# Performance work log

Measured on AMD Instinct MI355X. Metric: run time of the kernel, lower is better.

## Reference

```python
import jax, jax.numpy as jnp
import numpy as np

N_NODES = 100000
N_EDGES = 1600000
NFEAT, NHID, NCLASS = 64, 128, 32


def _glorot(key, shape):
    fan_in, fan_out = shape[0], shape[1]
    lim = np.sqrt(6.0 / (fan_in + fan_out))
    return jax.random.uniform(key, shape, jnp.float32, -lim, lim)


def setup_inputs() -> dict:
    key = jax.random.key(0)
    ks = jax.random.split(key, 12)
    x = jax.random.normal(ks[0], (N_NODES, NFEAT), jnp.float32)
    edge_idx = jax.random.randint(ks[1], (2, N_EDGES), 0, N_NODES, jnp.int64)
    edge_weight = jax.random.uniform(ks[2], (N_EDGES,), jnp.float32)
    return {
        "x": x,
        "edge_idx": edge_idx,
        "edge_weight": edge_weight,
        # SAGEConv 1: out = mean_agg(x) @ Wl1 + b1 + x @ Wr1
        "Wl1": _glorot(ks[3], (NFEAT, NHID)),
        "Wr1": _glorot(ks[4], (NFEAT, NHID)),
        "b1": jnp.zeros((NHID,), jnp.float32),
        # SAGEConv 2
        "Wl2": _glorot(ks[5], (NHID, NHID)),
        "Wr2": _glorot(ks[6], (NHID, NHID)),
        "b2": jnp.zeros((NHID,), jnp.float32),
        # fc head: Linear(nhid, nclass) -> Linear(nclass, 1)
        "Wfc1": _glorot(ks[7], (NHID, NCLASS)),
        "bfc1": jnp.zeros((NCLASS,), jnp.float32),
        "Wfc2": _glorot(ks[8], (NCLASS, 1)),
        "bfc2": jnp.zeros((1,), jnp.float32),
    }


def _sage_conv(x, src, dst, Wl, Wr, b, n_nodes):
    # mean aggregation of source features at destination nodes
    msg_sum = jax.ops.segment_sum(x[src], dst, num_segments=n_nodes)  # [N, d]
    deg = jax.ops.segment_sum(jnp.ones((src.shape[0], 1), x.dtype), dst,
                              num_segments=n_nodes)                    # [N, 1]
    mean = msg_sum / jnp.maximum(deg, 1.0)
    return mean @ Wl + b + x @ Wr


def reference(x, edge_idx, edge_weight, Wl1, Wr1, b1, Wl2, Wr2, b2,
              Wfc1, bfc1, Wfc2, bfc2):
    n_nodes = x.shape[0]
    src, dst = edge_idx[0], edge_idx[1]
    # dropout is identity in eval mode (training=False)
    h = _sage_conv(x, src, dst, Wl1, Wr1, b1, n_nodes)   # [N, nhid]
    h = _sage_conv(h, src, dst, Wl2, Wr2, b2, n_nodes)   # [N, nhid]
    h = h @ Wfc1 + bfc1                                   # [N, nclass]
    out = h @ Wfc2 + bfc2                                 # [N, 1]
    return out
```

## Files before the change

### kernel.cpp

```cpp
#include <hip/hip_runtime.h>

#define S_SHIFT 9
#define S_NODES 512
#define CAP     10240
#define CHUNK   4096
#define EPT     8
#define NREP    4

__global__ __launch_bounds__(512) void prep_kernel(
    const float* __restrict__ x,
    const int* __restrict__ src, const int* __restrict__ dst,
    int E, int N, int B,
    int* __restrict__ cursor, unsigned* __restrict__ bucket,
    const float* __restrict__ Wl1, const float* __restrict__ Wr1, const float* __restrict__ b1,
    const float* __restrict__ Wl2, const float* __restrict__ Wr2, const float* __restrict__ b2,
    const float* __restrict__ Wfc1, const float* __restrict__ bfc1,
    const float* __restrict__ Wfc2, const float* __restrict__ bfc2,
    float* __restrict__ ga, float2* __restrict__ gbc, float* __restrict__ c01)
{
    __shared__ unsigned stage[CHUNK];
    __shared__ unsigned char bn8[CHUNK];
    __shared__ int hist[256], scan[256], obase[256], lcur[256], lbase[256];
    __shared__ float wv[192], uu[128], vl2[128], vr2[128], w2[32];
    int t = threadIdx.x;
    int l = t & 63;
    int w = t >> 6;

    if (t < 32) w2[t] = Wfc2[t];
    __syncthreads();
    for (int j = 0; j < 16; ++j) {
        int i = w + 8 * j;
        float p = (l < 32) ? Wfc1[i * 32 + l] * w2[l] : 0.f;
        for (int m = 16; m; m >>= 1) p += __shfl_xor(p, m);
        if (l == 0) uu[i] = p;
    }
    __syncthreads();
    for (int j = 0; j < 16; ++j) {
        int i = w + 8 * j;
        float ua = uu[l], ub = uu[64 + l];
        float pa = Wl2[i * 128 + l] * ua + Wl2[i * 128 + 64 + l] * ub;
        float pb = Wr2[i * 128 + l] * ua + Wr2[i * 128 + 64 + l] * ub;
        for (int m = 32; m; m >>= 1) { pa += __shfl_xor(pa, m); pb += __shfl_xor(pb, m); }
        if (l == 0) { vl2[i] = pa; vr2[i] = pb; }
    }
    __syncthreads();
    for (int j = 0; j < 8; ++j) {
        int i = w + 8 * j;
        float l1a = Wl1[i * 128 + l], l1b = Wl1[i * 128 + 64 + l];
        float r1a = Wr1[i * 128 + l], r1b = Wr1[i * 128 + 64 + l];
        float La = vl2[l], Lb = vl2[64 + l], Ra = vr2[l], Rb = vr2[64 + l];
        float pc = l1a * La + l1b * Lb;
        float pb = l1a * Ra + l1b * Rb + r1a * La + r1b * Lb;
        float pa = r1a * Ra + r1b * Rb;
        for (int m = 32; m; m >>= 1) {
            pa += __shfl_xor(pa, m); pb += __shfl_xor(pb, m); pc += __shfl_xor(pc, m);
        }
        if (l == 0) { wv[i] = pa; wv[64 + i] = pb; wv[128 + i] = pc; }
    }
    if (blockIdx.x == 0 && w == 7) {
        float p0 = b1[l] * vr2[l] + b1[64 + l] * vr2[64 + l]
                 + b2[l] * uu[l] + b2[64 + l] * uu[64 + l];
        if (l < 32) p0 += bfc1[l] * w2[l];
        float p1 = b1[l] * vl2[l] + b1[64 + l] * vl2[64 + l];
        for (int m = 32; m; m >>= 1) { p0 += __shfl_xor(p0, m); p1 += __shfl_xor(p1, m); }
        if (l == 0) { c01[0] = p0 + bfc2[0]; c01[1] = p1; }
    }

    {
        int e0 = blockIdx.x * CHUNK;
        int cnt = E - e0; if (cnt > CHUNK) cnt = CHUNK;
        int sd[EPT], ss[EPT];
        if (t < 256) hist[t] = 0;
        __syncthreads();
        for (int k = 0; k < EPT; ++k) {
            int i = t + k * 512;
            if (i < cnt) {
                sd[k] = dst[e0 + i];
                ss[k] = src[e0 + i];
                atomicAdd(&hist[sd[k] >> S_SHIFT], 1);
            }
        }
        __syncthreads();
        if (t < 256) scan[t] = hist[t];
        __syncthreads();
        for (int off = 1; off < 256; off <<= 1) {
            int tmp = 0;
            if (t < 256 && t >= off) tmp = scan[t - off];
            __syncthreads();
            if (t < 256) scan[t] += tmp;
            __syncthreads();
        }
        if (t < 256) {
            int ob = scan[t] - hist[t];
            obase[t] = ob;
            lcur[t] = ob;
            if (t < B && hist[t] > 0) lbase[t] = atomicAdd(&cursor[t], hist[t]);
        }
        __syncthreads();
        for (int k = 0; k < EPT; ++k) {
            int i = t + k * 512;
            if (i < cnt) {
                int bb = sd[k] >> S_SHIFT;
                int pos = atomicAdd(&lcur[bb], 1);
                stage[pos] = ((unsigned)ss[k] << S_SHIFT) | (unsigned)(sd[k] & (S_NODES - 1));
                bn8[pos] = (unsigned char)bb;
            }
        }
        __syncthreads();
        for (int i = t; i < cnt; i += 512) {
            int bb = bn8[i];
            bucket[(size_t)bb * CAP + (unsigned)(lbase[bb] + (i - obase[bb]))] = stage[i];
        }
    }

    {
        int fp = l & 15, sub = l >> 4;
        float4 wa4 = ((const float4*)wv)[fp];
        float4 wb4 = ((const float4*)wv)[16 + fp];
        float4 wc4 = ((const float4*)wv)[32 + fp];
        const float4* x4 = (const float4*)x;
        int Q = (N + 3) >> 2;
        int stride = gridDim.x * 8;
        for (int qd = blockIdx.x * 8 + w; qd < Q; qd += stride) {
            int node = qd * 4 + sub;
            float a = 0.f, b = 0.f, c = 0.f;
            if (node < N) {
                float4 v = x4[(size_t)node * 16 + fp];
                a = v.x * wa4.x + v.y * wa4.y + v.z * wa4.z + v.w * wa4.w;
                b = v.x * wb4.x + v.y * wb4.y + v.z * wb4.z + v.w * wb4.w;
                c = v.x * wc4.x + v.y * wc4.y + v.z * wc4.z + v.w * wc4.w;
            }
            for (int m = 8; m; m >>= 1) {
                a += __shfl_xor(a, m); b += __shfl_xor(b, m); c += __shfl_xor(c, m);
            }
            if (fp == 0 && node < N) { ga[node] = a; gbc[node] = make_float2(b, c); }
        }
    }
}

__global__ __launch_bounds__(1024) void aggA_kernel(
    const unsigned* __restrict__ bucket, const int* __restrict__ cursor,
    const float2* __restrict__ gbc, const float* __restrict__ ga,
    const float* __restrict__ c01,
    float* __restrict__ q, float* __restrict__ t1, float* __restrict__ inv, int N)
{
    __shared__ float aB[NREP][S_NODES], aC[NREP][S_NODES];
    __shared__ int cnt[NREP][S_NODES];
    int t = threadIdx.x, b = blockIdx.x;
    int r = (t >> 6) & (NREP - 1);
    float* aBf = (float*)aB; float* aCf = (float*)aC; int* cnf = (int*)cnt;
    for (int i = t; i < NREP * S_NODES; i += 1024) { aBf[i] = 0.f; aCf[i] = 0.f; cnf[i] = 0; }
    __syncthreads();
    int n = cursor[b];
    const unsigned* bp = bucket + (size_t)b * CAP;
    for (int i = t; i < n; i += 1024) {
        unsigned uu = bp[i];
        float2 g = gbc[uu >> S_SHIFT];
        int dl = uu & (S_NODES - 1);
        atomicAdd(&aB[r][dl], g.x);
        atomicAdd(&aC[r][dl], g.y);
        atomicAdd(&cnt[r][dl], 1);
    }
    __syncthreads();
    if (t < S_NODES) {
        int node = (b << S_SHIFT) + t;
        if (node < N) {
            float sb = aB[0][t] + aB[1][t] + aB[2][t] + aB[3][t];
            float sc = aC[0][t] + aC[1][t] + aC[2][t] + aC[3][t];
            int d = cnt[0][t] + cnt[1][t] + cnt[2][t] + cnt[3][t];
            float iv = 1.0f / ((d > 0) ? (float)d : 1.0f);
            inv[node] = iv;
            q[node]   = iv * sc;
            t1[node]  = ga[node] + iv * sb + c01[0] + (d > 0 ? c01[1] : 0.f);
        }
    }
}

__global__ __launch_bounds__(1024) void aggB_kernel(
    const unsigned* __restrict__ bucket, const int* __restrict__ cursor,
    const float* __restrict__ q, const float* __restrict__ t1,
    const float* __restrict__ inv, float* __restrict__ out, int N)
{
    __shared__ float a2[NREP][S_NODES];
    int t = threadIdx.x, b = blockIdx.x;
    int r = (t >> 6) & (NREP - 1);
    float* a2f = (float*)a2;
    for (int i = t; i < NREP * S_NODES; i += 1024) a2f[i] = 0.f;
    __syncthreads();
    int n = cursor[b];
    const unsigned* bp = bucket + (size_t)b * CAP;
    for (int i = t; i < n; i += 1024) {
        unsigned uu = bp[i];
        atomicAdd(&a2[r][uu & (S_NODES - 1)], q[uu >> S_SHIFT]);
    }
    __syncthreads();
    if (t < S_NODES) {
        int node = (b << S_SHIFT) + t;
        if (node < N)
            out[node] = t1[node] + inv[node] * (a2[0][t] + a2[1][t] + a2[2][t] + a2[3][t]);
    }
}

extern "C" void kernel_launch(void* const* d_in, const int* in_sizes, int n_in,
                              void* d_out, int out_size, void* d_ws, size_t ws_size,
                              hipStream_t stream) {
    const float* x    = (const float*)d_in[0];
    const int*   eidx = (const int*)d_in[1];
    const float* Wl1  = (const float*)d_in[3];
    const float* Wr1  = (const float*)d_in[4];
    const float* b1   = (const float*)d_in[5];
    const float* Wl2  = (const float*)d_in[6];
    const float* Wr2  = (const float*)d_in[7];
    const float* b2   = (const float*)d_in[8];
    const float* Wfc1 = (const float*)d_in[9];
    const float* bfc1 = (const float*)d_in[10];
    const float* Wfc2 = (const float*)d_in[11];
    const float* bfc2 = (const float*)d_in[12];

    const int N = in_sizes[0] / 64;
    const int E = in_sizes[2];
    const int* src = eidx;
    const int* dst = eidx + E;
    const int B = (N + S_NODES - 1) / S_NODES;
    const int nprep = (E + CHUNK - 1) / CHUNK;

    char* ws = (char*)d_ws;
    int*      cursor = (int*)(ws);
    float*    c01    = (float*)(ws + 1024);
    float*    ga     = (float*)(ws + 2048);
    float*    q      = (float*)(ws + 2048 + (size_t)N * 4);
    float*    t1     = (float*)(ws + 2048 + (size_t)N * 8);
    float*    inv    = (float*)(ws + 2048 + (size_t)N * 12);
    float2*   gbc    = (float2*)(ws + 2048 + (size_t)N * 16);
    unsigned* bucket = (unsigned*)(ws + 2048 + (size_t)N * 24);

    hipMemsetAsync(cursor, 0, 1024, stream);

    prep_kernel<<<nprep, 512, 0, stream>>>(
        x, src, dst, E, N, B, cursor, bucket,
        Wl1, Wr1, b1, Wl2, Wr2, b2, Wfc1, bfc1, Wfc2, bfc2,
        ga, gbc, c01);

    aggA_kernel<<<B, 1024, 0, stream>>>(bucket, cursor, gbc, ga, c01, q, t1, inv, N);
    aggB_kernel<<<B, 1024, 0, stream>>>(bucket, cursor, q, t1, inv, (float*)d_out, N);
}
```

Measured before the change: 176.4 us.

## Split prep kernel warps into scatter and node-dot roles, drop LDS staging

Inside the prep kernel, warps 0-3 now bucket the edge chunk while warps 4-7 compute the per-node dot products, spread across the barrier phases so the two jobs overlap. The LDS staging buffer and prefix scan are removed, and each edge is written straight to its global bucket slot through a per-bucket shared atomic cursor. This cuts barriers and shared memory use, which may raise occupancy. In exchange, edge order within a bucket becomes non-deterministic, global writes are less coalesced, and each scatter thread handles twice as many edges.

Result: slower. 180.6 us (+2.4%).

```diff
diff --git a/kernel.cpp b/kernel.cpp
--- a/kernel.cpp
+++ b/kernel.cpp
@@ -4,7 +4,7 @@
 #define S_NODES 512
 #define CAP     10240
 #define CHUNK   4096
-#define EPT     8
+#define EPTS    16
 #define NREP    4
 
 __global__ __launch_bounds__(512) void prep_kernel(
@@ -18,9 +18,7 @@
     const float* __restrict__ Wfc2, const float* __restrict__ bfc2,
     float* __restrict__ ga, float2* __restrict__ gbc, float* __restrict__ c01)
 {
-    __shared__ unsigned stage[CHUNK];
-    __shared__ unsigned char bn8[CHUNK];
-    __shared__ int hist[256], scan[256], obase[256], lcur[256], lbase[256];
+    __shared__ int hist[256], lbase[256], lcur[256];
     __shared__ float wv[192], uu[128], vl2[128], vr2[128], w2[32];
     int t = threadIdx.x;
     int l = t & 63;
@@ -65,77 +63,80 @@
         for (int m = 32; m; m >>= 1) { p0 += __shfl_xor(p0, m); p1 += __shfl_xor(p1, m); }
         if (l == 0) { c01[0] = p0 + bfc2[0]; c01[1] = p1; }
     }
-
-    {
-        int e0 = blockIdx.x * CHUNK;
-        int cnt = E - e0; if (cnt > CHUNK) cnt = CHUNK;
-        int sd[EPT], ss[EPT];
-        if (t < 256) hist[t] = 0;
-        __syncthreads();
-        for (int k = 0; k < EPT; ++k) {
-            int i = t + k * 512;
+    __syncthreads();
+
+    bool is_scat = (w < 4);
+    int e0 = blockIdx.x * CHUNK;
+    int cnt = E - e0; if (cnt > CHUNK) cnt = CHUNK;
+    int sd[EPTS], ss[EPTS];
+
+    int fp = l & 15, sub = l >> 4;
+    float4 wa4, wb4, wc4;
+    int dbase = 0, dstride = 1, KT = 0, KPP = 0;
+    const float4* x4 = (const float4*)x;
+    int Q = (N + 3) >> 2;
+    if (!is_scat) {
+        wa4 = ((const float4*)wv)[fp];
+        wb4 = ((const float4*)wv)[16 + fp];
+        wc4 = ((const float4*)wv)[32 + fp];
+        dbase = blockIdx.x * 4 + (w - 4);
+        dstride = gridDim.x * 4;
+        KT = (Q - dbase + dstride - 1) / dstride;
+        if (KT < 0) KT = 0;
+        KPP = (KT + 3) >> 2;
+    }
+#define DOTS_PHASE(ph)                                                          \
+    if (!is_scat) {                                                             \
+        for (int k = (ph) * KPP; k < ((ph) + 1) * KPP && k < KT; ++k) {         \
+            int node = (dbase + k * dstride) * 4 + sub;                         \
+            float a = 0.f, b = 0.f, c = 0.f;                                    \
+            if (node < N) {                                                     \
+                float4 v = x4[(size_t)node * 16 + fp];                          \
+                a = v.x * wa4.x + v.y * wa4.y + v.z * wa4.z + v.w * wa4.w;      \
+                b = v.x * wb4.x + v.y * wb4.y + v.z * wb4.z + v.w * wb4.w;      \
+                c = v.x * wc4.x + v.y * wc4.y + v.z * wc4.z + v.w * wc4.w;      \
+            }                                                                   \
+            for (int m = 8; m; m >>= 1) {                                       \
+                a += __shfl_xor(a, m); b += __shfl_xor(b, m); c += __shfl_xor(c, m); \
+            }                                                                   \
+            if (fp == 0 && node < N) { ga[node] = a; gbc[node] = make_float2(b, c); } \
+        }                                                                       \
+    }
+
+    if (is_scat) hist[t] = 0;
+    DOTS_PHASE(0)
+    __syncthreads();
+    if (is_scat) {
+        for (int k = 0; k < EPTS; ++k) {
+            int i = t + k * 256;
             if (i < cnt) {
                 sd[k] = dst[e0 + i];
                 ss[k] = src[e0 + i];
                 atomicAdd(&hist[sd[k] >> S_SHIFT], 1);
             }
         }
-        __syncthreads();
-        if (t < 256) scan[t] = hist[t];
-        __syncthreads();
-        for (int off = 1; off < 256; off <<= 1) {
-            int tmp = 0;
-            if (t < 256 && t >= off) tmp = scan[t - off];
-            __syncthreads();
-            if (t < 256) scan[t] += tmp;
-            __syncthreads();
-        }
-        if (t < 256) {
-            int ob = scan[t] - hist[t];
-            obase[t] = ob;
-            lcur[t] = ob;
-            if (t < B && hist[t] > 0) lbase[t] = atomicAdd(&cursor[t], hist[t]);
-        }
-        __syncthreads();
-        for (int k = 0; k < EPT; ++k) {
-            int i = t + k * 512;
+    }
+    DOTS_PHASE(1)
+    __syncthreads();
+    if (is_scat) {
+        lcur[t] = 0;
+        if (t < B && hist[t] > 0) lbase[t] = atomicAdd(&cursor[t], hist[t]);
+    }
+    DOTS_PHASE(2)
+    __syncthreads();
+    if (is_scat) {
+        for (int k = 0; k < EPTS; ++k) {
+            int i = t + k * 256;
             if (i < cnt) {
                 int bb = sd[k] >> S_SHIFT;
-                int pos = atomicAdd(&lcur[bb], 1);
-                stage[pos] = ((unsigned)ss[k] << S_SHIFT) | (unsigned)(sd[k] & (S_NODES - 1));
-                bn8[pos] = (unsigned char)bb;
+                int off = atomicAdd(&lcur[bb], 1);
+                bucket[(size_t)bb * CAP + (unsigned)(lbase[bb] + off)] =
+                    ((unsigned)ss[k] << S_SHIFT) | (unsigned)(sd[k] & (S_NODES - 1));
             }
         }
-        __syncthreads();
-        for (int i = t; i < cnt; i += 512) {
-            int bb = bn8[i];
-            bucket[(size_t)bb * CAP + (unsigned)(lbase[bb] + (i - obase[bb]))] = stage[i];
-        }
-    }
-
-    {
-        int fp = l & 15, sub = l >> 4;
-        float4 wa4 = ((const float4*)wv)[fp];
-        float4 wb4 = ((const float4*)wv)[16 + fp];
-        float4 wc4 = ((const float4*)wv)[32 + fp];
-        const float4* x4 = (const float4*)x;
-        int Q = (N + 3) >> 2;
-        int stride = gridDim.x * 8;
-        for (int qd = blockIdx.x * 8 + w; qd < Q; qd += stride) {
-            int node = qd * 4 + sub;
-            float a = 0.f, b = 0.f, c = 0.f;
-            if (node < N) {
-                float4 v = x4[(size_t)node * 16 + fp];
-                a = v.x * wa4.x + v.y * wa4.y + v.z * wa4.z + v.w * wa4.w;
-                b = v.x * wb4.x + v.y * wb4.y + v.z * wb4.z + v.w * wb4.w;
-                c = v.x * wc4.x + v.y * wc4.y + v.z * wc4.z + v.w * wc4.w;
-            }
-            for (int m = 8; m; m >>= 1) {
-                a += __shfl_xor(a, m); b += __shfl_xor(b, m); c += __shfl_xor(c, m);
-            }
-            if (fp == 0 && node < N) { ga[node] = a; gbc[node] = make_float2(b, c); }
-        }
-    }
+    }
+    DOTS_PHASE(3)
+#undef DOTS_PHASE
 }
 
 __global__ __launch_bounds__(1024) void aggA_kernel(
```
